# Kernel optimization log

Measured on AMD Instinct MI355X. Metric: run time of the kernel, lower is better.

The kernel has to match this reference:

```python
import jax, jax.numpy as jnp
import numpy as np

NUM_ITERATIONS = 100
EPS = 1e-6
LIPSCHITZ_COEFF = 0.9


def _l2_normalize(x, axis=None, eps=1e-12):
    return x * jax.lax.rsqrt((x * x).sum(axis=axis, keepdims=True) + eps)


def setup_inputs() -> dict:
    key = jax.random.key(0)
    k1, k2, k3, k4 = jax.random.split(key, 4)
    B, D_in, D_out = 32768, 1024, 1024
    x = jax.random.normal(k1, (B, D_in), dtype=jnp.float32)
    # TruncatedNormal(stddev=1/sqrt(fan_in)) approximated by scaled normal
    w = jax.random.normal(k2, (D_in, D_out), dtype=jnp.float32) / np.sqrt(D_in)
    b = jax.random.normal(k3, (D_out,), dtype=jnp.float32)
    u0 = jax.random.normal(k4, (1, D_out), dtype=jnp.float32)
    return {"x": x, "w": w, "b": b, "u0": u0}


def reference(x, w, b, u0):
    d_in = w.shape[0]

    # 100-step power iteration: tight sequential dependency chain of GEMV pairs.
    def body(i, carry):
        u, _ = carry
        v = _l2_normalize(jnp.matmul(u, w.T), eps=EPS)   # [1, d_in]
        u = _l2_normalize(jnp.matmul(v, w), eps=EPS)     # [1, d_out]
        return (u, v)

    v_init = jnp.zeros((1, d_in), dtype=w.dtype)
    u, v = jax.lax.fori_loop(0, NUM_ITERATIONS, body, (u0, v_init))
    u = jax.lax.stop_gradient(u)
    v = jax.lax.stop_gradient(v)

    sigma = jnp.matmul(jnp.matmul(v, w), u.T)[0, 0]      # spectral norm estimate
    factor = jnp.maximum(1.0, sigma / LIPSCHITZ_COEFF)
    w_norm = w / factor

    out = jnp.dot(x, w_norm) + b
    return out
```

## Files before the change

kernel.cpp:

```cpp
#include <hip/hip_runtime.h>
#include <hip/hip_bf16.h>
#include <cstdint>
#include <cstddef>

#define DDIM 1024
#define BROWS 32768

typedef __attribute__((ext_vector_type(8))) short short8;
typedef __attribute__((ext_vector_type(4))) float floatx4;

__device__ __forceinline__ float bf2f(unsigned short u) {
  return __uint_as_float(((unsigned int)u) << 16);
}
__device__ __forceinline__ unsigned short f2bf(float f) {
  unsigned int u = __float_as_uint(f);
  u += 0x7FFFu + ((u >> 16) & 1u);
  return (unsigned short)(u >> 16);
}

__device__ __forceinline__ void load_lds16(const void* g, void* l) {
  __builtin_amdgcn_global_load_lds(
      (const __attribute__((address_space(1))) unsigned int*)g,
      (__attribute__((address_space(3))) unsigned int*)l,
      16, 0, 0);
}

__global__ void __launch_bounds__(256, 4)
big_gemm(const float* __restrict__ Af, const unsigned short* __restrict__ Bt,
         float* __restrict__ Outf, const float* __restrict__ inv_ptr,
         const float* __restrict__ bias)
{
  __shared__ __align__(16) char smem[16896];
  unsigned short* As = (unsigned short*)smem;
  unsigned short* Bs = (unsigned short*)(smem + 8192);
  float* epi = (float*)smem;

  const int tid  = threadIdx.x;
  const int lane = tid & 63;
  const int wid  = tid >> 6;
  const int wr = wid >> 1, wc = wid & 1;
  const int g = lane >> 4, r = lane & 15;

  const int bm0 = (int)(blockIdx.x & 255) * 128;
  const int bn0 = (int)(blockIdx.x >> 8) * 128;

  const floatx4 zero4 = {0.f, 0.f, 0.f, 0.f};
  floatx4 acc[4][4];
#pragma unroll
  for (int m = 0; m < 4; ++m)
#pragma unroll
    for (int n = 0; n < 4; ++n) acc[m][n] = zero4;

  for (int kk = 0; kk < DDIM; kk += 32) {
    __syncthreads();
#pragma unroll
    for (int p = 0; p < 2; ++p) {
      const int o = p * 4096 + tid * 16;
      const int row = o >> 6;
      const int cole = (o & 63) >> 1;
      load_lds16(Bt + (size_t)(bn0 + row) * DDIM + kk + cole, (char*)Bs + o);
    }
#pragma unroll
    for (int p = 0; p < 2; ++p) {
      const int o = p * 4096 + tid * 16;
      const int row = o >> 6;
      const int cole = (o & 63) >> 1;
      const float4* s = (const float4*)(Af + (size_t)(bm0 + row) * DDIM + kk + cole);
      float4 x0 = s[0], x1 = s[1];
      short8 t;
      t[0] = (short)f2bf(x0.x); t[1] = (short)f2bf(x0.y);
      t[2] = (short)f2bf(x0.z); t[3] = (short)f2bf(x0.w);
      t[4] = (short)f2bf(x1.x); t[5] = (short)f2bf(x1.y);
      t[6] = (short)f2bf(x1.z); t[7] = (short)f2bf(x1.w);
      *(short8*)((char*)As + o) = t;
    }
    __syncthreads();

    short8 afr[4], bfr[4];
#pragma unroll
    for (int m = 0; m < 4; ++m)
      afr[m] = *(const short8*)((const char*)As + (wr * 64 + m * 16 + r) * 64 + g * 16);
#pragma unroll
    for (int n = 0; n < 4; ++n)
      bfr[n] = *(const short8*)((const char*)Bs + (wc * 64 + n * 16 + r) * 64 + g * 16);
#pragma unroll
    for (int m = 0; m < 4; ++m)
#pragma unroll
      for (int n = 0; n < 4; ++n)
        acc[m][n] = __builtin_amdgcn_mfma_f32_16x16x32_bf16(afr[m], bfr[n], acc[m][n], 0, 0, 0);
  }

  const float inv = *inv_ptr;
  float bv[4];
#pragma unroll
  for (int n = 0; n < 4; ++n) bv[n] = bias[bn0 + wc * 64 + n * 16 + r];

#pragma unroll
  for (int m = 0; m < 4; ++m) {
    __syncthreads();
#pragma unroll
    for (int n = 0; n < 4; ++n)
#pragma unroll
      for (int q = 0; q < 4; ++q)
        epi[(wr * 16 + g * 4 + q) * 132 + wc * 64 + n * 16 + r] =
            acc[m][n][q] * inv + bv[n];
    __syncthreads();
    const int lrow = tid >> 3;
    const int lc0  = (tid & 7) * 16;
    const int grow = bm0 + m * 16 + (lrow & 15) + (lrow >> 4) * 64;
    float4* dst = (float4*)(Outf + (size_t)grow * DDIM + bn0 + lc0);
    const float4* sv = (const float4*)(epi + lrow * 132 + lc0);
    dst[0] = sv[0]; dst[1] = sv[1]; dst[2] = sv[2]; dst[3] = sv[3];
  }
}

__global__ void __launch_bounds__(256, 2)
sq_gemm(const unsigned short* __restrict__ A, const unsigned short* __restrict__ Bt,
        unsigned short* __restrict__ Out, const float* __restrict__ in_max,
        float* __restrict__ out_max)
{
  __shared__ __align__(16) unsigned short As[2][4096];
  __shared__ __align__(16) unsigned short Bs[2][4096];
  __shared__ float redw[4];

  const int tid  = threadIdx.x;
  const int lane = tid & 63;
  const int wid  = tid >> 6;
  const int wr = wid >> 1, wc = wid & 1;
  const int g = lane >> 4, r = lane & 15;

  const int bm0 = (int)(blockIdx.x >> 4) * 64;
  const int bn0 = (int)(blockIdx.x & 15) * 64;

  const int so    = tid * 16;
  const int srow0 = so >> 7;
  const int sc16  = (so >> 4) & 7;
  const int scs   = sc16 ^ (srow0 & 7);
  const unsigned short* aSrc0 = A  + (size_t)(bm0 + srow0) * DDIM + scs * 8;
  const unsigned short* aSrc1 = A  + (size_t)(bm0 + 32 + srow0) * DDIM + scs * 8;
  const unsigned short* bSrc0 = Bt + (size_t)(bn0 + srow0) * DDIM + scs * 8;
  const unsigned short* bSrc1 = Bt + (size_t)(bn0 + 32 + srow0) * DDIM + scs * 8;

  const floatx4 zero4 = {0.f, 0.f, 0.f, 0.f};
  floatx4 acc[2][2];
#pragma unroll
  for (int fm = 0; fm < 2; ++fm)
#pragma unroll
    for (int fn = 0; fn < 2; ++fn) acc[fm][fn] = zero4;

  load_lds16(aSrc0, (char*)&As[0][0] + so);
  load_lds16(aSrc1, (char*)&As[0][0] + 4096 + so);
  load_lds16(bSrc0, (char*)&Bs[0][0] + so);
  load_lds16(bSrc1, (char*)&Bs[0][0] + 4096 + so);
  __syncthreads();

  int buf = 0;
  for (int t = 0; t < 16; ++t) {
    if (t + 1 < 16) {
      const int kk = (t + 1) * 64;
      load_lds16(aSrc0 + kk, (char*)&As[buf ^ 1][0] + so);
      load_lds16(aSrc1 + kk, (char*)&As[buf ^ 1][0] + 4096 + so);
      load_lds16(bSrc0 + kk, (char*)&Bs[buf ^ 1][0] + so);
      load_lds16(bSrc1 + kk, (char*)&Bs[buf ^ 1][0] + 4096 + so);
    }
#pragma unroll
    for (int ks = 0; ks < 2; ++ks) {
      const int chunk = ((ks << 2) + g) ^ (r & 7);
      short8 af[2], bf[2];
#pragma unroll
      for (int fm = 0; fm < 2; ++fm) {
        const int arow = wr * 32 + fm * 16 + r;
        af[fm] = *(const short8*)((const char*)&As[buf][0] + (arow << 7) + (chunk << 4));
      }
#pragma unroll
      for (int fn = 0; fn < 2; ++fn) {
        const int brow = wc * 32 + fn * 16 + r;
        bf[fn] = *(const short8*)((const char*)&Bs[buf][0] + (brow << 7) + (chunk << 4));
      }
#pragma unroll
      for (int fm = 0; fm < 2; ++fm)
#pragma unroll
        for (int fn = 0; fn < 2; ++fn)
          acc[fm][fn] = __builtin_amdgcn_mfma_f32_16x16x32_bf16(af[fm], bf[fn], acc[fm][fn], 0, 0, 0);
    }
    __syncthreads();
    buf ^= 1;
  }

  float c = 1.0f;
  if (in_max != nullptr) {
    int e;
    (void)frexpf(*in_max, &e);
    c = ldexpf(1.0f, -e);
  }
  const float c2 = c * c;
  float lmax = 0.0f;
#pragma unroll
  for (int fm = 0; fm < 2; ++fm) {
#pragma unroll
    for (int fn = 0; fn < 2; ++fn) {
      const int ocol = bn0 + wc * 32 + fn * 16 + r;
#pragma unroll
      for (int q = 0; q < 4; ++q) {
        const int orow = bm0 + wr * 32 + fm * 16 + g * 4 + q;
        float v = acc[fm][fn][q] * c2;
        Out[(size_t)orow * DDIM + ocol] = f2bf(v);
        lmax = fmaxf(lmax, fabsf(v));
      }
    }
  }
#pragma unroll
  for (int off = 32; off > 0; off >>= 1) lmax = fmaxf(lmax, __shfl_down(lmax, off));
  if (lane == 0) redw[wid] = lmax;
  __syncthreads();
  if (tid == 0) {
    float m = fmaxf(fmaxf(redw[0], redw[1]), fmaxf(redw[2], redw[3]));
    atomicMax((unsigned int*)out_max, __float_as_uint(m));
  }
}

__global__ void __launch_bounds__(256)
transpose_bf16(const float* __restrict__ W, unsigned short* __restrict__ WT)
{
  __shared__ float tile[64][65];
  const int bx = blockIdx.x & 15;
  const int by = blockIdx.x >> 4;
  const int tid = threadIdx.x;
  const int c = tid & 63;
  const int r0 = tid >> 6;
#pragma unroll
  for (int p = 0; p < 16; ++p) {
    int kr = p * 4 + r0;
    tile[kr][c] = W[(size_t)(bx * 64 + kr) * DDIM + by * 64 + c];
  }
  __syncthreads();
#pragma unroll
  for (int p = 0; p < 16; ++p) {
    int nr = p * 4 + r0;
    WT[(size_t)(by * 64 + nr) * DDIM + bx * 64 + c] = f2bf(tile[c][nr]);
  }
}

__global__ void __launch_bounds__(256)
gemv_pow(const unsigned short* __restrict__ P, const float* __restrict__ vin,
         float* __restrict__ vout)
{
  const int tid = threadIdx.x;
  const int lane = tid & 63;
  const int wid = tid >> 6;
  float vs[16];
  const float4* vv = (const float4*)(vin + lane * 16);
#pragma unroll
  for (int i = 0; i < 4; ++i) {
    float4 t = vv[i];
    vs[i * 4 + 0] = t.x; vs[i * 4 + 1] = t.y; vs[i * 4 + 2] = t.z; vs[i * 4 + 3] = t.w;
  }
#pragma unroll
  for (int rr = 0; rr < 4; ++rr) {
    const int row = (int)blockIdx.x * 16 + wid * 4 + rr;
    const unsigned short* pr = P + (size_t)row * DDIM + lane * 16;
    short8 p0 = *(const short8*)pr;
    short8 p1 = *(const short8*)(pr + 8);
    float s = 0.f;
#pragma unroll
    for (int e = 0; e < 8; ++e) s += bf2f((unsigned short)p0[e]) * vs[e];
#pragma unroll
    for (int e = 0; e < 8; ++e) s += bf2f((unsigned short)p1[e]) * vs[8 + e];
#pragma unroll
    for (int off = 32; off > 0; off >>= 1) s += __shfl_down(s, off);
    if (lane == 0) vout[row] = s * 0x1p-12f;
  }
}

__global__ void __launch_bounds__(256)
v_kernel(const float* __restrict__ W, const float* __restrict__ d,
         float* __restrict__ v_un, float* __restrict__ vpart)
{
  __shared__ float wsum[4];
  const int tid = threadIdx.x;
  const int lane = tid & 63;
  const int wid = tid >> 6;
  float vs[16];
  const float4* dv = (const float4*)(d + lane * 16);
#pragma unroll
  for (int i = 0; i < 4; ++i) {
    float4 t = dv[i];
    vs[i * 4 + 0] = t.x; vs[i * 4 + 1] = t.y; vs[i * 4 + 2] = t.z; vs[i * 4 + 3] = t.w;
  }
  float ssq = 0.f;
#pragma unroll
  for (int rr = 0; rr < 4; ++rr) {
    const int row = (int)blockIdx.x * 16 + wid * 4 + rr;
    const float4* wrow = (const float4*)(W + (size_t)row * DDIM + lane * 16);
    float s = 0.f;
#pragma unroll
    for (int i = 0; i < 4; ++i) {
      float4 t = wrow[i];
      s += t.x * vs[i * 4 + 0] + t.y * vs[i * 4 + 1] + t.z * vs[i * 4 + 2] + t.w * vs[i * 4 + 3];
    }
#pragma unroll
    for (int off = 32; off > 0; off >>= 1) s += __shfl_down(s, off);
    if (lane == 0) { v_un[row] = s; ssq += s * s; }
  }
  if (lane == 0) wsum[wid] = ssq;
  __syncthreads();
  if (tid == 0) vpart[blockIdx.x] = (wsum[0] + wsum[1]) + (wsum[2] + wsum[3]);
}

__global__ void __launch_bounds__(256)
t_fin_kernel(const float* __restrict__ W, const float* __restrict__ v_un,
             float* __restrict__ vpart, float* __restrict__ tpart,
             unsigned int* __restrict__ counter, float* __restrict__ inv_out)
{
  __shared__ float part[8][33];
  __shared__ unsigned int sticket;
  const int tid = threadIdx.x;
  const int col = (int)blockIdx.x * 32 + (tid & 31);
  const int ch = tid >> 5;
  float s = 0.f;
  const int i0 = ch * 128;
  for (int i = i0; i < i0 + 128; ++i)
    s += v_un[i] * W[(size_t)i * DDIM + col];
  part[ch][tid & 31] = s;
  __syncthreads();
  if (tid < 32) {
    float t = 0.f;
#pragma unroll
    for (int c2 = 0; c2 < 8; ++c2) t += part[c2][tid];
    part[0][tid] = t * t;
  }
  __syncthreads();
  if (tid == 0) {
    float ss = 0.f;
#pragma unroll
    for (int c = 0; c < 32; ++c) ss += part[0][c];
    tpart[blockIdx.x] = ss;
    __threadfence();
    sticket = atomicAdd(counter, 1u);
  }
  __syncthreads();
  if (sticket == 31) {
    __threadfence();
    float val = 0.f;
    if (tid < 64)
      val = __uint_as_float(atomicOr((unsigned int*)&vpart[tid], 0u));
    part[tid >> 5][tid & 31] = val;
    __syncthreads();
    if (tid == 0) {
      float sv = 0.f;
      for (int i = 0; i < 64; ++i) sv += part[i >> 5][i & 31];
      float stq = 0.f;
      for (int i = 0; i < 32; ++i)
        stq += __uint_as_float(atomicOr((unsigned int*)&tpart[i], 0u));
      float sigma = sqrtf(stq / sv);
      inv_out[0] = (sigma > 0.9f) ? (0.9f / sigma) : 1.0f;
    }
  }
}

extern "C" void kernel_launch(void* const* d_in, const int* in_sizes, int n_in,
                              void* d_out, int out_size, void* d_ws, size_t ws_size,
                              hipStream_t stream)
{
  const float* x  = (const float*)d_in[0];
  const float* w  = (const float*)d_in[1];
  const float* b  = (const float*)d_in[2];
  const float* u0 = (const float*)d_in[3];
  float* out = (float*)d_out;

  char* ws = (char*)d_ws;
  float* scal = (float*)ws;
  float* u_a  = (float*)(ws + 0x1000);
  float* u_b  = (float*)(ws + 0x2000);
  float* v_un = (float*)(ws + 0x3000);
  unsigned short* WT = (unsigned short*)(ws + 0x4000);
  unsigned short* P0 = (unsigned short*)(ws + 0x204000);
  unsigned short* P1 = (unsigned short*)(ws + 0x404000);

  hipMemsetAsync(d_ws, 0, 4096, stream);
  hipLaunchKernelGGL(transpose_bf16, dim3(256), dim3(256), 0, stream, w, WT);

  hipLaunchKernelGGL(sq_gemm, dim3(256), dim3(256), 0, stream,
                     WT, WT, P0, (const float*)nullptr, &scal[0]);
  hipLaunchKernelGGL(sq_gemm, dim3(256), dim3(256), 0, stream,
                     P0, P0, P1, &scal[0], &scal[1]);
  hipLaunchKernelGGL(sq_gemm, dim3(256), dim3(256), 0, stream,
                     P1, P1, P0, &scal[1], &scal[2]);
  hipLaunchKernelGGL(sq_gemm, dim3(256), dim3(256), 0, stream,
                     P0, P0, P1, &scal[2], &scal[3]);
  hipLaunchKernelGGL(sq_gemm, dim3(256), dim3(256), 0, stream,
                     P1, P1, P0, &scal[3], &scal[4]);
  hipLaunchKernelGGL(sq_gemm, dim3(256), dim3(256), 0, stream,
                     P0, P0, P1, &scal[4], &scal[5]);

  hipLaunchKernelGGL(gemv_pow, dim3(64), dim3(256), 0, stream, P1, u0, u_a);
  hipLaunchKernelGGL(gemv_pow, dim3(64), dim3(256), 0, stream, P1, u_a, u_b);
  hipLaunchKernelGGL(gemv_pow, dim3(64), dim3(256), 0, stream, P1, u_b, u_a);

  hipLaunchKernelGGL(v_kernel, dim3(64), dim3(256), 0, stream, w, u_a, v_un, &scal[16]);
  hipLaunchKernelGGL(t_fin_kernel, dim3(32), dim3(256), 0, stream,
                     w, v_un, &scal[16], &scal[80],
                     (unsigned int*)&scal[120], &scal[8]);

  hipLaunchKernelGGL(big_gemm, dim3(2048), dim3(256), 0, stream,
                     x, WT, out, &scal[8], b);
}
```

Before: 271.8 us.

## Keep a 64-row bf16 A panel resident in LDS and stream W tiles

```diff
diff --git a/kernel.cpp b/kernel.cpp
--- a/kernel.cpp
+++ b/kernel.cpp
@@ -25,92 +25,111 @@
       16, 0, 0);
 }
 
-__global__ void __launch_bounds__(256, 4)
-big_gemm(const float* __restrict__ Af, const unsigned short* __restrict__ Bt,
-         float* __restrict__ Outf, const float* __restrict__ inv_ptr,
-         const float* __restrict__ bias)
-{
-  __shared__ __align__(16) char smem[16896];
-  unsigned short* As = (unsigned short*)smem;
-  unsigned short* Bs = (unsigned short*)(smem + 8192);
-  float* epi = (float*)smem;
+__global__ void __launch_bounds__(512)
+big_gemm_pa(const float* __restrict__ Af, const unsigned short* __restrict__ Bt,
+            float* __restrict__ Outf, const float* __restrict__ inv_ptr,
+            const float* __restrict__ bias)
+{
+  __shared__ __align__(16) char Asm[131072];
+  __shared__ __align__(16) char Bsm[2 * 8192];
 
   const int tid  = threadIdx.x;
   const int lane = tid & 63;
-  const int wid  = tid >> 6;
-  const int wr = wid >> 1, wc = wid & 1;
+  const int w    = tid >> 6;
+  const int wm = w >> 2, wn = w & 3;
   const int g = lane >> 4, r = lane & 15;
-
-  const int bm0 = (int)(blockIdx.x & 255) * 128;
-  const int bn0 = (int)(blockIdx.x >> 8) * 128;
-
-  const floatx4 zero4 = {0.f, 0.f, 0.f, 0.f};
-  floatx4 acc[4][4];
-#pragma unroll
-  for (int m = 0; m < 4; ++m)
-#pragma unroll
-    for (int n = 0; n < 4; ++n) acc[m][n] = zero4;
-
-  for (int kk = 0; kk < DDIM; kk += 32) {
+  const int gm = (int)blockIdx.x * 64;
+
+#pragma unroll
+  for (int p = 0; p < 16; ++p) {
+    const int idx = p * 4096 + tid * 8;
+    const int row = idx >> 10;
+    const int col = idx & 1023;
+    const float4* s = (const float4*)(Af + (size_t)(gm + row) * DDIM + col);
+    float4 x0 = s[0], x1 = s[1];
+    short8 t;
+    t[0] = (short)f2bf(x0.x); t[1] = (short)f2bf(x0.y);
+    t[2] = (short)f2bf(x0.z); t[3] = (short)f2bf(x0.w);
+    t[4] = (short)f2bf(x1.x); t[5] = (short)f2bf(x1.y);
+    t[6] = (short)f2bf(x1.z); t[7] = (short)f2bf(x1.w);
+    const int pc = (col >> 3) ^ (row & 7);
+    *(short8*)(Asm + row * 2048 + pc * 16) = t;
+  }
+  const float inv = *inv_ptr;
+  __syncthreads();
+
+  const int brow = tid >> 2;
+  const int bsc  = (tid & 3) ^ (brow & 3);
+
+  for (int nit = 0; nit < 8; ++nit) {
+    const int n0 = nit * 128;
+    const unsigned short* bbase = Bt + (size_t)(n0 + brow) * DDIM + bsc * 8;
+
+    const floatx4 zero4 = {0.f, 0.f, 0.f, 0.f};
+    floatx4 acc[2][2];
+#pragma unroll
+    for (int i = 0; i < 2; ++i)
+#pragma unroll
+      for (int j = 0; j < 2; ++j) acc[i][j] = zero4;
+
+    load_lds16(bbase, Bsm + tid * 16);
     __syncthreads();
-#pragma unroll
-    for (int p = 0; p < 2; ++p) {
-      const int o = p * 4096 + tid * 16;
-      const int row = o >> 6;
-      const int cole = (o & 63) >> 1;
-      load_lds16(Bt + (size_t)(bn0 + row) * DDIM + kk + cole, (char*)Bs + o);
-    }
-#pragma unroll
-    for (int p = 0; p < 2; ++p) {
-      const int o = p * 4096 + tid * 16;
-      const int row = o >> 6;
-      const int cole = (o & 63) >> 1;
-      const float4* s = (const float4*)(Af + (size_t)(bm0 + row) * DDIM + kk + cole);
-      float4 x0 = s[0], x1 = s[1];
-      short8 t;
-      t[0] = (short)f2bf(x0.x); t[1] = (short)f2bf(x0.y);
-      t[2] = (short)f2bf(x0.z); t[3] = (short)f2bf(x0.w);
-      t[4] = (short)f2bf(x1.x); t[5] = (short)f2bf(x1.y);
-      t[6] = (short)f2bf(x1.z); t[7] = (short)f2bf(x1.w);
-      *(short8*)((char*)As + o) = t;
-    }
-    __syncthreads();
-
-    short8 afr[4], bfr[4];
-#pragma unroll
-    for (int m = 0; m < 4; ++m)
-      afr[m] = *(const short8*)((const char*)As + (wr * 64 + m * 16 + r) * 64 + g * 16);
-#pragma unroll
-    for (int n = 0; n < 4; ++n)
-      bfr[n] = *(const short8*)((const char*)Bs + (wc * 64 + n * 16 + r) * 64 + g * 16);
-#pragma unroll
-    for (int m = 0; m < 4; ++m)
-#pragma unroll
-      for (int n = 0; n < 4; ++n)
-        acc[m][n] = __builtin_amdgcn_mfma_f32_16x16x32_bf16(afr[m], bfr[n], acc[m][n], 0, 0, 0);
-  }
-
-  const float inv = *inv_ptr;
-  float bv[4];
-#pragma unroll
-  for (int n = 0; n < 4; ++n) bv[n] = bias[bn0 + wc * 64 + n * 16 + r];
-
-#pragma unroll
-  for (int m = 0; m < 4; ++m) {
-    __syncthreads();
-#pragma unroll
-    for (int n = 0; n < 4; ++n)
-#pragma unroll
-      for (int q = 0; q < 4; ++q)
-        epi[(wr * 16 + g * 4 + q) * 132 + wc * 64 + n * 16 + r] =
-            acc[m][n][q] * inv + bv[n];
-    __syncthreads();
-    const int lrow = tid >> 3;
-    const int lc0  = (tid & 7) * 16;
-    const int grow = bm0 + m * 16 + (lrow & 15) + (lrow >> 4) * 64;
-    float4* dst = (float4*)(Outf + (size_t)grow * DDIM + bn0 + lc0);
-    const float4* sv = (const float4*)(epi + lrow * 132 + lc0);
-    dst[0] = sv[0]; dst[1] = sv[1]; dst[2] = sv[2]; dst[3] = sv[3];
+
+    int buf = 0;
+    for (int t = 0; t < 32; ++t) {
+      if (t + 1 < 32)
+        load_lds16(bbase + (t + 1) * 32, Bsm + ((buf ^ 1) << 13) + tid * 16);
+
+      short8 af[2], bf[2];
+#pragma unroll
+      for (int i = 0; i < 2; ++i) {
+        const int arow = wm * 32 + i * 16 + r;
+        const int kc = ((t << 2) + g) ^ (r & 7);
+        af[i] = *(const short8*)(Asm + arow * 2048 + kc * 16);
+      }
+#pragma unroll
+      for (int j = 0; j < 2; ++j) {
+        const int br = wn * 32 + j * 16 + r;
+        const int bc = g ^ (r & 3);
+        bf[j] = *(const short8*)(Bsm + (buf << 13) + br * 64 + bc * 16);
+      }
+#pragma unroll
+      for (int i = 0; i < 2; ++i)
+#pragma unroll
+        for (int j = 0; j < 2; ++j)
+          acc[i][j] = __builtin_amdgcn_mfma_f32_16x16x32_bf16(af[i], bf[j], acc[i][j], 0, 0, 0);
+
+      __syncthreads();
+      buf ^= 1;
+    }
+
+    float bj[2];
+#pragma unroll
+    for (int j = 0; j < 2; ++j) bj[j] = bias[n0 + wn * 32 + j * 16 + r];
+    float* epi = (float*)Bsm;
+#pragma unroll
+    for (int h = 0; h < 2; ++h) {
+      if (wm == h) {
+#pragma unroll
+        for (int i = 0; i < 2; ++i)
+#pragma unroll
+          for (int j = 0; j < 2; ++j)
+#pragma unroll
+            for (int q = 0; q < 4; ++q)
+              epi[(i * 16 + g * 4 + q) * 128 + wn * 32 + j * 16 + r] =
+                  acc[i][j][q] * inv + bj[j];
+      }
+      __syncthreads();
+      {
+        const int row32 = tid >> 4;
+        const int col0  = (tid & 15) * 8;
+        const float4* sv = (const float4*)(epi + row32 * 128 + col0);
+        float4 v0 = sv[0], v1 = sv[1];
+        float4* dst = (float4*)(Outf + (size_t)(gm + h * 32 + row32) * DDIM + n0 + col0);
+        dst[0] = v0; dst[1] = v1;
+      }
+      __syncthreads();
+    }
   }
 }
 
@@ -402,6 +421,6 @@
                      w, v_un, &scal[16], &scal[80],
                      (unsigned int*)&scal[120], &scal[8]);
 
-  hipLaunchKernelGGL(big_gemm, dim3(2048), dim3(256), 0, stream,
+  hipLaunchKernelGGL(big_gemm_pa, dim3(512), dim3(512), 0, stream,
                      x, WT, out, &scal[8], b);
 }
```

New measurement: 339.0 us. 1.25x slower.
